# Kernel optimization log

Measured on AMD Instinct MI355X. Metric: run time of the kernel, lower is better.

Reference implementation:

```python
import jax, jax.numpy as jnp
import numpy as np
import math

NUM_LAYERS_HALF = 2   # num_layers // 2
NUM_HEADS = 12
DIM = 768
FFN_DIM = 3072
VOCAB = 50257
BLOCK = 2048
LN_EPS = 1e-5


def _sinusoidal_pe(max_len, dim):
    pos = np.arange(max_len, dtype=np.float32)[:, None]
    div = np.exp(np.arange(0, dim, 2, dtype=np.float32) * (-math.log(10000.0) / dim))
    pe = np.zeros((max_len, dim), dtype=np.float32)
    pe[:, 0::2] = np.sin(pos * div)
    pe[:, 1::2] = np.cos(pos * div)
    return jnp.asarray(pe)[None]  # [1, max_len, dim]


def setup_inputs() -> dict:
    key = jax.random.key(0)
    ks = jax.random.split(key, 16)
    L, D, F = NUM_LAYERS_HALF, DIM, FFN_DIM
    s = 0.02
    return {
        "idx": jax.random.randint(ks[0], (1, 2048), 0, VOCAB),
        "token_emb": jax.random.normal(ks[1], (VOCAB, D), jnp.float32) * s,
        "pe": _sinusoidal_pe(BLOCK, D),
        "qkv_w": jax.random.normal(ks[2], (L, D, 3 * D), jnp.float32) * s,
        "qkv_b": jnp.zeros((L, 3 * D), jnp.float32),
        "out_w": jax.random.normal(ks[3], (L, D, D), jnp.float32) * s,
        "out_b": jnp.zeros((L, D), jnp.float32),
        "ln1_s": jnp.ones((L, D), jnp.float32),
        "ln1_b": jnp.zeros((L, D), jnp.float32),
        "ln2_s": jnp.ones((L, D), jnp.float32),
        "ln2_b": jnp.zeros((L, D), jnp.float32),
        "w1": jax.random.normal(ks[4], (L, D, F), jnp.float32) * s,
        "b1": jnp.zeros((L, F), jnp.float32),
        "w2": jax.random.normal(ks[5], (L, F, D), jnp.float32) * s,
        "b2": jnp.zeros((L, D), jnp.float32),
    }


def _layer_norm(x, scale, bias):
    m = jnp.mean(x, axis=-1, keepdims=True)
    v = jnp.mean(jnp.square(x - m), axis=-1, keepdims=True)
    return (x - m) * jax.lax.rsqrt(v + LN_EPS) * scale + bias


def _forward(idx, token_emb, pe, qkv_w, qkv_b, out_w, out_b,
             ln1_s, ln1_b, ln2_s, ln2_b, w1, b1, w2, b2):
    B, S = idx.shape
    D, H = DIM, NUM_HEADS
    hd = D // H
    x = token_emb[idx] + pe[:, :S]                     # [B,S,D]
    causal = jnp.tril(jnp.ones((S, S), dtype=bool))    # [S,S]

    def block(x, p):
        qw, qb, ow, ob, l1s, l1b, l2s, l2b, fw1, fb1, fw2, fb2 = p
        h = _layer_norm(x, l1s, l1b)
        qkv = (h @ qw + qb).reshape(B, S, 3, H, hd)
        q, k, v = jnp.moveaxis(qkv, 2, 0)              # each [B,S,H,hd]
        q = q.transpose(0, 2, 1, 3)                    # [B,H,S,hd]
        k = k.transpose(0, 2, 1, 3)
        v = v.transpose(0, 2, 1, 3)
        scores = jnp.einsum('bhqd,bhkd->bhqk', q, k) / math.sqrt(hd)
        scores = jnp.where(causal, scores, -1e9)
        attn = jax.nn.softmax(scores, axis=-1)
        o = jnp.einsum('bhqk,bhkd->bhqd', attn, v)
        o = o.transpose(0, 2, 1, 3).reshape(B, S, D)
        x = x + (o @ ow + ob)
        h2 = _layer_norm(x, l2s, l2b)
        ff = jax.nn.gelu(h2 @ fw1 + fb1, approximate=False) @ fw2 + fb2
        return x + ff, None

    params = (qkv_w, qkv_b, out_w, out_b, ln1_s, ln1_b, ln2_s, ln2_b, w1, b1, w2, b2)
    x, _ = jax.lax.scan(block, x, params)
    return x


def reference(idx, token_emb, pe, qkv_w, qkv_b, out_w, out_b,
              ln1_s, ln1_b, ln2_s, ln2_b, w1, b1, w2, b2):
    return _forward(idx, token_emb, pe, qkv_w, qkv_b, out_w, out_b,
                    ln1_s, ln1_b, ln2_s, ln2_b, w1, b1, w2, b2)
```

## Files before the change

kernel.cpp:

```cpp
#include <hip/hip_runtime.h>
#include <hip/hip_bf16.h>


#define SEQ 2048
#define DIM 768
#define NH 12
#define HD 64
#define FFN 3072
#define QKVD (3 * DIM)

typedef __attribute__((ext_vector_type(8))) short short8;
typedef __attribute__((ext_vector_type(4))) float f32x4;

__device__ __forceinline__ ushort bf16bits(float v) {
    __hip_bfloat16 hb = __float2bfloat16(v);
    return *reinterpret_cast<ushort*>(&hb);
}

__device__ __forceinline__ void gload_lds16(const ushort* g, ushort* l) {
    __builtin_amdgcn_global_load_lds(
        (const __attribute__((address_space(1))) void*)g,
        (__attribute__((address_space(3))) void*)l, 16, 0, 0);
}

__global__ void embed_kernel(const int* __restrict__ idx,
                             const float* __restrict__ emb,
                             const float* __restrict__ pe,
                             float* __restrict__ x) {
    int i = blockIdx.x * 256 + threadIdx.x;
    int s = i / DIM;
    int d = i - s * DIM;
    x[i] = emb[idx[s] * DIM + d] + pe[i];
}

__global__ void transpose_w(const float* __restrict__ W,
                            __hip_bfloat16* __restrict__ WT, int K, int N) {
    __shared__ float t[32][33];
    const float* Wp = W + (size_t)blockIdx.z * K * N;
    __hip_bfloat16* Tp = WT + (size_t)blockIdx.z * K * N;
    int k0 = blockIdx.y * 32, n0 = blockIdx.x * 32;
    int r = threadIdx.x >> 3, c4 = (threadIdx.x & 7) * 4;
    float4 v = *(const float4*)&Wp[(size_t)(k0 + r) * N + n0 + c4];
    t[r][c4 + 0] = v.x; t[r][c4 + 1] = v.y; t[r][c4 + 2] = v.z; t[r][c4 + 3] = v.w;
    __syncthreads();
    __hip_bfloat16* dst = &Tp[(size_t)(n0 + r) * K + k0 + c4];
#pragma unroll
    for (int j = 0; j < 4; ++j) dst[j] = __float2bfloat16(t[c4 + j][r]);
}

__global__ void ln_kernel(const float* __restrict__ x,
                          const float* __restrict__ sc,
                          const float* __restrict__ bi,
                          __hip_bfloat16* __restrict__ h) {
    int row = blockIdx.x, tid = threadIdx.x;
    __shared__ float red[256];
    const float* xr = x + row * DIM;
    float v[3];
#pragma unroll
    for (int i = 0; i < 3; ++i) v[i] = xr[tid + i * 256];
    float s = v[0] + v[1] + v[2];
    red[tid] = s; __syncthreads();
    for (int t = 128; t > 0; t >>= 1) {
        if (tid < t) red[tid] += red[tid + t];
        __syncthreads();
    }
    float mean = red[0] * (1.0f / DIM);
    __syncthreads();
    float q = 0.f;
#pragma unroll
    for (int i = 0; i < 3; ++i) { float d = v[i] - mean; q += d * d; }
    red[tid] = q; __syncthreads();
    for (int t = 128; t > 0; t >>= 1) {
        if (tid < t) red[tid] += red[tid + t];
        __syncthreads();
    }
    float rstd = rsqrtf(red[0] * (1.0f / DIM) + 1e-5f);
#pragma unroll
    for (int i = 0; i < 3; ++i) {
        int d = tid + i * 256;
        h[row * DIM + d] = __float2bfloat16((v[i] - mean) * rstd * sc[d] + bi[d]);
    }
}

template <int BN, bool GELU, bool RES, bool OUTBF16>
__global__ __launch_bounds__(256) void mfma_gemm(
        const ushort* __restrict__ A, const ushort* __restrict__ WT,
        const float* __restrict__ bias, const float* __restrict__ res,
        void* __restrict__ Cout, int M, int N, int K) {
    constexpr int NT = BN / 32;
    __shared__ ushort As[128 * 32];
    __shared__ ushort Bs[BN * 32];
    int tid = threadIdx.x;
    int w = tid >> 6, lane = tid & 63;
    int wm = (w >> 1) * 64, wn = (w & 1) * (BN / 2);
    int bm = blockIdx.y * 128, bn = blockIdx.x * BN;
    int lm = lane & 15, q8 = (lane >> 4) * 8;

    f32x4 acc[4][NT];
#pragma unroll
    for (int i = 0; i < 4; ++i)
#pragma unroll
        for (int j = 0; j < NT; ++j) acc[i][j] = {0.f, 0.f, 0.f, 0.f};

    int c0 = tid, c1 = tid + 256;
    const ushort* pa0 = &A[(size_t)(bm + (c0 >> 2)) * K + (c0 & 3) * 8];
    const ushort* pa1 = &A[(size_t)(bm + (c1 >> 2)) * K + (c1 & 3) * 8];
    const ushort* pb0 = &WT[(size_t)(bn + (c0 >> 2)) * K + (c0 & 3) * 8];
    const ushort* pb1 = nullptr;
    if constexpr (BN == 128)
        pb1 = &WT[(size_t)(bn + (c1 >> 2)) * K + (c1 & 3) * 8];

    for (int k0 = 0; k0 < K; k0 += 32) {
        __syncthreads();
        gload_lds16(pa0 + k0, &As[c0 * 8]);
        gload_lds16(pa1 + k0, &As[c1 * 8]);
        gload_lds16(pb0 + k0, &Bs[c0 * 8]);
        if constexpr (BN == 128)
            gload_lds16(pb1 + k0, &Bs[c1 * 8]);
        __syncthreads();

        short8 af[4], bw[NT];
#pragma unroll
        for (int mt = 0; mt < 4; ++mt)
            af[mt] = *(const short8*)&As[(wm + mt * 16 + lm) * 32 + q8];
#pragma unroll
        for (int nt = 0; nt < NT; ++nt)
            bw[nt] = *(const short8*)&Bs[(wn + nt * 16 + lm) * 32 + q8];
#pragma unroll
        for (int mt = 0; mt < 4; ++mt)
#pragma unroll
            for (int nt = 0; nt < NT; ++nt)
                acc[mt][nt] = __builtin_amdgcn_mfma_f32_16x16x32_bf16(
                    af[mt], bw[nt], acc[mt][nt], 0, 0, 0);
    }

#pragma unroll
    for (int nt = 0; nt < NT; ++nt) {
        int col = bn + wn + nt * 16 + lm;
        float bv = bias[col];
#pragma unroll
        for (int mt = 0; mt < 4; ++mt) {
            int rowb = bm + wm + mt * 16 + (q8 >> 1);
#pragma unroll
            for (int r = 0; r < 4; ++r) {
                int row = rowb + r;
                float v = acc[mt][nt][r] + bv;
                if (GELU) v = 0.5f * v * (1.0f + erff(v * 0.70710678118654752f));
                if (RES) v += res[(size_t)row * N + col];
                if (OUTBF16)
                    ((__hip_bfloat16*)Cout)[(size_t)row * N + col] = __float2bfloat16(v);
                else
                    ((float*)Cout)[(size_t)row * N + col] = v;
            }
        }
    }
}

__global__ __launch_bounds__(256) void flash_attn_kernel(
        const ushort* __restrict__ qkv, ushort* __restrict__ o) {
    int pair = blockIdx.x, head = blockIdx.y;
    int tid = threadIdx.x, w = tid >> 6, lane = tid & 63;
    int ln16 = lane & 15, quad = lane >> 4;

    __shared__ ushort Ks[64 * 72];
    __shared__ ushort Vt[64 * 72];
    __shared__ ushort Ps[4][16 * 72];

#pragma unroll 1
    for (int ph = 0; ph < 2; ++ph) {
        int qt = ph ? (31 - pair) : pair;

        short8 qf[2];
        {
            const ushort* qp = &qkv[(size_t)(qt * 64 + w * 16 + ln16) * QKVD
                                    + head * HD + quad * 8];
            qf[0] = *(const short8*)qp;
            qf[1] = *(const short8*)(qp + 32);
        }

        float m_i = -1e30f, l_i = 0.f;
        f32x4 oacc[4];
#pragma unroll
        for (int mt = 0; mt < 4; ++mt) oacc[mt] = {0.f, 0.f, 0.f, 0.f};

        for (int kt = 0; kt <= qt; ++kt) {
            __syncthreads();
#pragma unroll
            for (int hh = 0; hh < 2; ++hh) {
                int t = hh * 256 + tid;
                int key = t >> 3, c8 = (t & 7) * 8;
                const ushort* kp = &qkv[(size_t)(kt * 64 + key) * QKVD + DIM
                                        + head * HD + c8];
                *(short8*)&Ks[key * 72 + c8] = *(const short8*)kp;
                short8 vv = *(const short8*)(kp + DIM);
#pragma unroll
                for (int j = 0; j < 8; ++j)
                    Vt[(c8 + j) * 72 + key] = ((const ushort*)&vv)[j];
            }
            __syncthreads();

            f32x4 s[4];
#pragma unroll
            for (int mt = 0; mt < 4; ++mt) {
                s[mt] = {0.f, 0.f, 0.f, 0.f};
#pragma unroll
                for (int kc = 0; kc < 2; ++kc) {
                    short8 kf = *(const short8*)&Ks[(mt * 16 + ln16) * 72
                                                    + kc * 32 + quad * 8];
                    s[mt] = __builtin_amdgcn_mfma_f32_16x16x32_bf16(
                        kf, qf[kc], s[mt], 0, 0, 0);
                }
            }

            int qrow = qt * 64 + w * 16 + ln16;
            float sv[4][4];
#pragma unroll
            for (int mt = 0; mt < 4; ++mt)
#pragma unroll
                for (int r = 0; r < 4; ++r) {
                    float v = s[mt][r] * 0.125f;
                    int key = kt * 64 + mt * 16 + quad * 4 + r;
                    sv[mt][r] = (kt == qt && key > qrow) ? -1e30f : v;
                }

            float tmax = -1e30f;
#pragma unroll
            for (int mt = 0; mt < 4; ++mt)
#pragma unroll
                for (int r = 0; r < 4; ++r) tmax = fmaxf(tmax, sv[mt][r]);
            tmax = fmaxf(tmax, __shfl_xor(tmax, 16));
            tmax = fmaxf(tmax, __shfl_xor(tmax, 32));
            float m_new = fmaxf(m_i, tmax);
            float alpha = __expf(m_i - m_new);
            m_i = m_new;

            float ls = 0.f;
#pragma unroll
            for (int mt = 0; mt < 4; ++mt) {
                union { ushort u[4]; unsigned long long ull; } pk;
#pragma unroll
                for (int r = 0; r < 4; ++r) {
                    float p = __expf(sv[mt][r] - m_new);
                    ls += p;
                    pk.u[r] = bf16bits(p);
                }
                *(unsigned long long*)&Ps[w][ln16 * 72 + mt * 16 + quad * 4] = pk.ull;
            }
            ls += __shfl_xor(ls, 16);
            ls += __shfl_xor(ls, 32);
            l_i = l_i * alpha + ls;

#pragma unroll
            for (int mt = 0; mt < 4; ++mt) {
                oacc[mt][0] *= alpha; oacc[mt][1] *= alpha;
                oacc[mt][2] *= alpha; oacc[mt][3] *= alpha;
            }

#pragma unroll
            for (int kc = 0; kc < 2; ++kc) {
                short8 pf = *(const short8*)&Ps[w][ln16 * 72 + kc * 32 + quad * 8];
#pragma unroll
                for (int mt = 0; mt < 4; ++mt) {
                    short8 vf = *(const short8*)&Vt[(mt * 16 + ln16) * 72
                                                    + kc * 32 + quad * 8];
                    oacc[mt] = __builtin_amdgcn_mfma_f32_16x16x32_bf16(
                        vf, pf, oacc[mt], 0, 0, 0);
                }
            }
        }

        float inv = 1.0f / l_i;
        int orow = qt * 64 + w * 16 + ln16;
#pragma unroll
        for (int mt = 0; mt < 4; ++mt)
#pragma unroll
            for (int r = 0; r < 4; ++r) {
                int dimc = head * HD + mt * 16 + quad * 4 + r;
                o[(size_t)orow * DIM + dimc] = bf16bits(oacc[mt][r] * inv);
            }
    }
}

extern "C" void kernel_launch(void* const* d_in, const int* in_sizes, int n_in,
                              void* d_out, int out_size, void* d_ws, size_t ws_size,
                              hipStream_t stream) {
    const int*   idx   = (const int*)  d_in[0];
    const float* emb   = (const float*)d_in[1];
    const float* pe    = (const float*)d_in[2];
    const float* qkv_w = (const float*)d_in[3];
    const float* qkv_b = (const float*)d_in[4];
    const float* out_w = (const float*)d_in[5];
    const float* out_b = (const float*)d_in[6];
    const float* ln1_s = (const float*)d_in[7];
    const float* ln1_b = (const float*)d_in[8];
    const float* ln2_s = (const float*)d_in[9];
    const float* ln2_b = (const float*)d_in[10];
    const float* w1    = (const float*)d_in[11];
    const float* b1    = (const float*)d_in[12];
    const float* w2    = (const float*)d_in[13];
    const float* b2    = (const float*)d_in[14];

    float* x = (float*)d_ws;
    __hip_bfloat16* h   = (__hip_bfloat16*)(x + SEQ * DIM);
    __hip_bfloat16* qkv = h + SEQ * DIM;
    __hip_bfloat16* ffa = qkv + (size_t)SEQ * QKVD;
    __hip_bfloat16* qkv_wT = ffa + (size_t)SEQ * FFN;
    __hip_bfloat16* out_wT = qkv_wT + (size_t)2 * QKVD * DIM;
    __hip_bfloat16* w1T    = out_wT + (size_t)2 * DIM * DIM;
    __hip_bfloat16* w2T    = w1T + (size_t)2 * FFN * DIM;

    transpose_w<<<dim3(QKVD / 32, DIM / 32, 2), 256, 0, stream>>>(qkv_w, qkv_wT, DIM, QKVD);
    transpose_w<<<dim3(DIM / 32, DIM / 32, 2), 256, 0, stream>>>(out_w, out_wT, DIM, DIM);
    transpose_w<<<dim3(FFN / 32, DIM / 32, 2), 256, 0, stream>>>(w1, w1T, DIM, FFN);
    transpose_w<<<dim3(DIM / 32, FFN / 32, 2), 256, 0, stream>>>(w2, w2T, FFN, DIM);

    embed_kernel<<<SEQ * DIM / 256, 256, 0, stream>>>(idx, emb, pe, x);

    for (int l = 0; l < 2; ++l) {
        ln_kernel<<<SEQ, 256, 0, stream>>>(x, ln1_s + l * DIM, ln1_b + l * DIM, h);
        mfma_gemm<128, false, false, true><<<dim3(QKVD / 128, SEQ / 128), 256, 0, stream>>>(
            (const ushort*)h, (const ushort*)(qkv_wT + (size_t)l * QKVD * DIM),
            qkv_b + l * QKVD, nullptr, qkv, SEQ, QKVD, DIM);
        flash_attn_kernel<<<dim3(16, NH), 256, 0, stream>>>(
            (const ushort*)qkv, (ushort*)h);
        mfma_gemm<64, false, true, false><<<dim3(DIM / 64, SEQ / 128), 256, 0, stream>>>(
            (const ushort*)h, (const ushort*)(out_wT + (size_t)l * DIM * DIM),
            out_b + l * DIM, x, x, SEQ, DIM, DIM);
        ln_kernel<<<SEQ, 256, 0, stream>>>(x, ln2_s + l * DIM, ln2_b + l * DIM, h);
        mfma_gemm<128, true, false, true><<<dim3(FFN / 128, SEQ / 128), 256, 0, stream>>>(
            (const ushort*)h, (const ushort*)(w1T + (size_t)l * FFN * DIM),
            b1 + l * FFN, nullptr, ffa, SEQ, FFN, DIM);
        float* cdst = (l == 1) ? (float*)d_out : x;
        mfma_gemm<64, false, true, false><<<dim3(DIM / 64, SEQ / 128), 256, 0, stream>>>(
            (const ushort*)ffa, (const ushort*)(w2T + (size_t)l * DIM * FFN),
            b2 + l * DIM, x, cdst, SEQ, DIM, FFN);
    }
}
```

Before: 624.9 us.

## Double-buffer K/V in flash attention with one query tile per block

Flash attention now launches one block per (query tile, head), 384 blocks instead of 192 paired blocks, scheduling the longest tiles first. K/V tiles are double-buffered in shared memory, with the next tile's global loads issued before the current tile's compute, leaving one barrier per iteration. The V transpose buffer drops its padding in favour of an XOR swizzle to avoid bank conflicts, and the causal mask is applied only on the diagonal tile. This hides global-load latency and improves occupancy and balance, at the cost of more shared memory and registers per block.

New measurement: 617.3 us. No clear change (-1.2%).

```diff
diff --git a/kernel.cpp b/kernel.cpp
--- a/kernel.cpp
+++ b/kernel.cpp
@@ -158,127 +158,172 @@
 
 __global__ __launch_bounds__(256) void flash_attn_kernel(
         const ushort* __restrict__ qkv, ushort* __restrict__ o) {
-    int pair = blockIdx.x, head = blockIdx.y;
+    int bi = blockIdx.x;
+    int qt = 31 - bi / NH, head = bi % NH;
     int tid = threadIdx.x, w = tid >> 6, lane = tid & 63;
     int ln16 = lane & 15, quad = lane >> 4;
 
-    __shared__ ushort Ks[64 * 72];
-    __shared__ ushort Vt[64 * 72];
+    __shared__ ushort Ks[2][64 * 72];
+    __shared__ ushort Vt[2][64 * 64];
     __shared__ ushort Ps[4][16 * 72];
 
-#pragma unroll 1
-    for (int ph = 0; ph < 2; ++ph) {
-        int qt = ph ? (31 - pair) : pair;
-
-        short8 qf[2];
-        {
-            const ushort* qp = &qkv[(size_t)(qt * 64 + w * 16 + ln16) * QKVD
-                                    + head * HD + quad * 8];
-            qf[0] = *(const short8*)qp;
-            qf[1] = *(const short8*)(qp + 32);
-        }
-
-        float m_i = -1e30f, l_i = 0.f;
-        f32x4 oacc[4];
-#pragma unroll
-        for (int mt = 0; mt < 4; ++mt) oacc[mt] = {0.f, 0.f, 0.f, 0.f};
-
-        for (int kt = 0; kt <= qt; ++kt) {
-            __syncthreads();
+    int skey[2], sc8;
+    sc8 = (tid & 7) * 8;
+    skey[0] = tid >> 3;
+    skey[1] = (256 + tid) >> 3;
+
+    short8 kst[2], vst[2];
+    const ushort* kbase = qkv + DIM + head * HD + sc8;
+
+    short8 qf[2];
+    {
+        const ushort* qp = &qkv[(size_t)(qt * 64 + w * 16 + ln16) * QKVD
+                                + head * HD + quad * 8];
+        qf[0] = *(const short8*)qp;
+        qf[1] = *(const short8*)(qp + 32);
+    }
+
+#pragma unroll
+    for (int hh = 0; hh < 2; ++hh) {
+        const ushort* kp = kbase + (size_t)(0 * 64 + skey[hh]) * QKVD;
+        kst[hh] = *(const short8*)kp;
+        vst[hh] = *(const short8*)(kp + DIM);
+    }
+#pragma unroll
+    for (int hh = 0; hh < 2; ++hh) {
+        int key = skey[hh];
+        *(short8*)&Ks[0][key * 72 + sc8] = kst[hh];
+        int g0 = key >> 3, ke = key & 7;
+#pragma unroll
+        for (int j = 0; j < 8; ++j) {
+            int r = sc8 + j;
+            Vt[0][r * 64 + ((g0 ^ (r >> 3)) & 7) * 8 + ke] = ((ushort*)&vst[hh])[j];
+        }
+    }
+    __syncthreads();
+
+    float m_i = -1e30f, l_i = 0.f;
+    f32x4 oacc[4];
+#pragma unroll
+    for (int mt = 0; mt < 4; ++mt) oacc[mt] = {0.f, 0.f, 0.f, 0.f};
+
+    int cur = 0;
+    for (int kt = 0; kt <= qt; ++kt) {
+        bool pre = (kt < qt);
+        if (pre) {
 #pragma unroll
             for (int hh = 0; hh < 2; ++hh) {
-                int t = hh * 256 + tid;
-                int key = t >> 3, c8 = (t & 7) * 8;
-                const ushort* kp = &qkv[(size_t)(kt * 64 + key) * QKVD + DIM
-                                        + head * HD + c8];
-                *(short8*)&Ks[key * 72 + c8] = *(const short8*)kp;
-                short8 vv = *(const short8*)(kp + DIM);
-#pragma unroll
-                for (int j = 0; j < 8; ++j)
-                    Vt[(c8 + j) * 72 + key] = ((const ushort*)&vv)[j];
-            }
-            __syncthreads();
-
-            f32x4 s[4];
+                const ushort* kp = kbase + (size_t)((kt + 1) * 64 + skey[hh]) * QKVD;
+                kst[hh] = *(const short8*)kp;
+                vst[hh] = *(const short8*)(kp + DIM);
+            }
+        }
+
+        f32x4 s[4];
+#pragma unroll
+        for (int mt = 0; mt < 4; ++mt) {
+            s[mt] = {0.f, 0.f, 0.f, 0.f};
+#pragma unroll
+            for (int kc = 0; kc < 2; ++kc) {
+                short8 kf = *(const short8*)&Ks[cur][(mt * 16 + ln16) * 72
+                                                     + kc * 32 + quad * 8];
+                s[mt] = __builtin_amdgcn_mfma_f32_16x16x32_bf16(
+                    kf, qf[kc], s[mt], 0, 0, 0);
+            }
+        }
+
+        int qrow = qt * 64 + w * 16 + ln16;
+        float sv[4][4];
+        if (kt == qt) {
+#pragma unroll
+            for (int mt = 0; mt < 4; ++mt)
+#pragma unroll
+                for (int r = 0; r < 4; ++r) {
+                    int key = kt * 64 + mt * 16 + quad * 4 + r;
+                    sv[mt][r] = (key > qrow) ? -1e30f : s[mt][r] * 0.125f;
+                }
+        } else {
+#pragma unroll
+            for (int mt = 0; mt < 4; ++mt)
+#pragma unroll
+                for (int r = 0; r < 4; ++r) sv[mt][r] = s[mt][r] * 0.125f;
+        }
+
+        float tmax = -1e30f;
+#pragma unroll
+        for (int mt = 0; mt < 4; ++mt)
+#pragma unroll
+            for (int r = 0; r < 4; ++r) tmax = fmaxf(tmax, sv[mt][r]);
+        tmax = fmaxf(tmax, __shfl_xor(tmax, 16));
+        tmax = fmaxf(tmax, __shfl_xor(tmax, 32));
+        float m_new = fmaxf(m_i, tmax);
+        float alpha = __expf(m_i - m_new);
+        m_i = m_new;
+
+        float ls = 0.f;
+#pragma unroll
+        for (int mt = 0; mt < 4; ++mt) {
+            union { ushort u[4]; unsigned long long ull; } pk;
+#pragma unroll
+            for (int r = 0; r < 4; ++r) {
+                float p = __expf(sv[mt][r] - m_new);
+                ls += p;
+                pk.u[r] = bf16bits(p);
+            }
+            *(unsigned long long*)&Ps[w][ln16 * 72 + mt * 16 + quad * 4] = pk.ull;
+        }
+        ls += __shfl_xor(ls, 16);
+        ls += __shfl_xor(ls, 32);
+        l_i = l_i * alpha + ls;
+
+#pragma unroll
+        for (int mt = 0; mt < 4; ++mt) {
+            oacc[mt][0] *= alpha; oacc[mt][1] *= alpha;
+            oacc[mt][2] *= alpha; oacc[mt][3] *= alpha;
+        }
+
+#pragma unroll
+        for (int kc = 0; kc < 2; ++kc) {
+            short8 pf = *(const short8*)&Ps[w][ln16 * 72 + kc * 32 + quad * 8];
 #pragma unroll
             for (int mt = 0; mt < 4; ++mt) {
-                s[mt] = {0.f, 0.f, 0.f, 0.f};
-#pragma unroll
-                for (int kc = 0; kc < 2; ++kc) {
-                    short8 kf = *(const short8*)&Ks[(mt * 16 + ln16) * 72
-                                                    + kc * 32 + quad * 8];
-                    s[mt] = __builtin_amdgcn_mfma_f32_16x16x32_bf16(
-                        kf, qf[kc], s[mt], 0, 0, 0);
+                int row = mt * 16 + ln16;
+                int g = kc * 4 + quad;
+                short8 vf = *(const short8*)&Vt[cur][row * 64
+                                                     + ((g ^ (row >> 3)) & 7) * 8];
+                oacc[mt] = __builtin_amdgcn_mfma_f32_16x16x32_bf16(
+                    vf, pf, oacc[mt], 0, 0, 0);
+            }
+        }
+
+        if (pre) {
+            int nb = cur ^ 1;
+#pragma unroll
+            for (int hh = 0; hh < 2; ++hh) {
+                int key = skey[hh];
+                *(short8*)&Ks[nb][key * 72 + sc8] = kst[hh];
+                int g0 = key >> 3, ke = key & 7;
+#pragma unroll
+                for (int j = 0; j < 8; ++j) {
+                    int r = sc8 + j;
+                    Vt[nb][r * 64 + ((g0 ^ (r >> 3)) & 7) * 8 + ke] =
+                        ((ushort*)&vst[hh])[j];
                 }
             }
-
-            int qrow = qt * 64 + w * 16 + ln16;
-            float sv[4][4];
-#pragma unroll
-            for (int mt = 0; mt < 4; ++mt)
-#pragma unroll
-                for (int r = 0; r < 4; ++r) {
-                    float v = s[mt][r] * 0.125f;
-                    int key = kt * 64 + mt * 16 + quad * 4 + r;
-                    sv[mt][r] = (kt == qt && key > qrow) ? -1e30f : v;
-                }
-
-            float tmax = -1e30f;
-#pragma unroll
-            for (int mt = 0; mt < 4; ++mt)
-#pragma unroll
-                for (int r = 0; r < 4; ++r) tmax = fmaxf(tmax, sv[mt][r]);
-            tmax = fmaxf(tmax, __shfl_xor(tmax, 16));
-            tmax = fmaxf(tmax, __shfl_xor(tmax, 32));
-            float m_new = fmaxf(m_i, tmax);
-            float alpha = __expf(m_i - m_new);
-            m_i = m_new;
-
-            float ls = 0.f;
-#pragma unroll
-            for (int mt = 0; mt < 4; ++mt) {
-                union { ushort u[4]; unsigned long long ull; } pk;
-#pragma unroll
-                for (int r = 0; r < 4; ++r) {
-                    float p = __expf(sv[mt][r] - m_new);
-                    ls += p;
-                    pk.u[r] = bf16bits(p);
-                }
-                *(unsigned long long*)&Ps[w][ln16 * 72 + mt * 16 + quad * 4] = pk.ull;
-            }
-            ls += __shfl_xor(ls, 16);
-            ls += __shfl_xor(ls, 32);
-            l_i = l_i * alpha + ls;
-
-#pragma unroll
-            for (int mt = 0; mt < 4; ++mt) {
-                oacc[mt][0] *= alpha; oacc[mt][1] *= alpha;
-                oacc[mt][2] *= alpha; oacc[mt][3] *= alpha;
-            }
-
-#pragma unroll
-            for (int kc = 0; kc < 2; ++kc) {
-                short8 pf = *(const short8*)&Ps[w][ln16 * 72 + kc * 32 + quad * 8];
-#pragma unroll
-                for (int mt = 0; mt < 4; ++mt) {
-                    short8 vf = *(const short8*)&Vt[(mt * 16 + ln16) * 72
-                                                    + kc * 32 + quad * 8];
-                    oacc[mt] = __builtin_amdgcn_mfma_f32_16x16x32_bf16(
-                        vf, pf, oacc[mt], 0, 0, 0);
-                }
-            }
-        }
-
-        float inv = 1.0f / l_i;
-        int orow = qt * 64 + w * 16 + ln16;
-#pragma unroll
-        for (int mt = 0; mt < 4; ++mt)
-#pragma unroll
-            for (int r = 0; r < 4; ++r) {
-                int dimc = head * HD + mt * 16 + quad * 4 + r;
-                o[(size_t)orow * DIM + dimc] = bf16bits(oacc[mt][r] * inv);
-            }
-    }
+        }
+        __syncthreads();
+        cur ^= 1;
+    }
+
+    float inv = 1.0f / l_i;
+    int orow = qt * 64 + w * 16 + ln16;
+#pragma unroll
+    for (int mt = 0; mt < 4; ++mt)
+#pragma unroll
+        for (int r = 0; r < 4; ++r) {
+            int dimc = head * HD + mt * 16 + quad * 4 + r;
+            o[(size_t)orow * DIM + dimc] = bf16bits(oacc[mt][r] * inv);
+        }
 }
 
 extern "C" void kernel_launch(void* const* d_in, const int* in_sizes, int n_in,
@@ -321,7 +366,7 @@
         mfma_gemm<128, false, false, true><<<dim3(QKVD / 128, SEQ / 128), 256, 0, stream>>>(
             (const ushort*)h, (const ushort*)(qkv_wT + (size_t)l * QKVD * DIM),
             qkv_b + l * QKVD, nullptr, qkv, SEQ, QKVD, DIM);
-        flash_attn_kernel<<<dim3(16, NH), 256, 0, stream>>>(
+        flash_attn_kernel<<<dim3(32 * NH), 256, 0, stream>>>(
             (const ushort*)qkv, (ushort*)h);
         mfma_gemm<64, false, true, false><<<dim3(DIM / 64, SEQ / 128), 256, 0, stream>>>(
             (const ushort*)h, (const ushort*)(out_wT + (size_t)l * DIM * DIM),
```
